# Kernel optimization log

Measured on AMD Instinct MI355X. Metric: run time of the kernel, lower is better.

The kernel has to match this reference:

```python
import jax, jax.numpy as jnp
import numpy as np

PI_2 = 3.14159 / 2  # matches torch module constant (not exact pi/2, keeps tan finite)
EPS_SUM = 1e-07
EPS_COS = 1e-08  # torch F.cosine_similarity default eps


def setup_inputs() -> dict:
    key = jax.random.key(0)
    k1, k2 = jax.random.split(key)
    B, N, C, H, W = 16, 2000, 512, 7, 7
    # memory is uniform-initialized then sum-normalized per cube, as in __init__
    memory = jax.random.uniform(k1, (N, C, H, W), dtype=jnp.float32)
    memory = memory / (jnp.sum(memory, axis=(1, 2, 3), keepdims=True) + EPS_SUM)
    key_t = jax.random.uniform(k2, (B, C, H, W), dtype=jnp.float32)
    return {"key": key_t, "memory": memory}


def reference(key, memory):
    # _normalize: divide key by its per-sample sum
    k = key / (jnp.sum(key, axis=(1, 2, 3), keepdims=True) + EPS_SUM)
    B = k.shape[0]
    N = memory.shape[0]
    kf = k.reshape(B, -1)            # [B, D], D = C*H*W
    mf = memory.reshape(N, -1)       # [N, D]
    # cosine similarity (torch clamps each norm to eps)
    dots = jnp.einsum('bd,nd->bn', kf, mf)                       # [B, N]
    kn = jnp.maximum(jnp.linalg.norm(kf, axis=-1), EPS_COS)      # [B]
    mn = jnp.maximum(jnp.linalg.norm(mf, axis=-1), EPS_COS)      # [N]
    cos = dots / (kn[:, None] * mn[None, :])
    w = jax.nn.softmax(jnp.tan(cos * PI_2), axis=1)              # [B, N]
    # read: sum over memory cubes weighted by address w
    return jnp.einsum('bn,nchw->bchw', w, memory)                # [B, C, H, W]
```

## Files before the change

### kernel.cpp

```cpp
#include <hip/hip_runtime.h>
#include <hip/hip_fp16.h>
#include <math.h>

#define B 16
#define N 2000
#define D 25088
#define D4 6272
#define PI2 1.570795f
#define KC 28
#define KSPAN (D / KC)
#define KTILES (KSPAN / 32)
#define NT (D / 32)
#define KBLK (NT / 4)
#define NCHUNK 20
#define NPER (N / NCHUNK)
#define SELHI 0x07060302u
#define PSCALE 1048576.0f
#define PINV   (1.0f / 1048576.0f)

typedef __attribute__((ext_vector_type(8))) short short8;
typedef __attribute__((ext_vector_type(4))) float f32x4;
typedef unsigned int uint;

union pk { uint4 u; short8 s; };
__device__ __forceinline__ short8 as_s8(uint4 u) { pk p; p.u = u; return p.s; }
union hpk { __half2 h; uint u; };

__device__ __forceinline__ float wave_sum(float v) {
#pragma unroll
    for (int off = 32; off > 0; off >>= 1) v += __shfl_xor(v, off, 64);
    return v;
}
__device__ __forceinline__ float wave_max(float v) {
#pragma unroll
    for (int off = 32; off > 0; off >>= 1) v = fmaxf(v, __shfl_xor(v, off, 64));
    return v;
}

__device__ __forceinline__ void cvt_hilo(const float4& a, const float4& b,
                                         short8& hi, short8& lo, float4& msqv) {
    float xs[8] = {a.x, a.y, a.z, a.w, b.x, b.y, b.z, b.w};
    float* mq = &msqv.x;
    uint lu[8];
#pragma unroll
    for (int j = 0; j < 8; ++j) {
        uint u = __float_as_uint(xs[j]);
        float lof = xs[j] - __uint_as_float(u & 0xffff0000u);
        lu[j] = __float_as_uint(lof);
        mq[j & 3] = fmaf(xs[j], xs[j], mq[j & 3]);
    }
    uint4 h, l;
    h.x = __builtin_amdgcn_perm(__float_as_uint(xs[1]), __float_as_uint(xs[0]), SELHI);
    h.y = __builtin_amdgcn_perm(__float_as_uint(xs[3]), __float_as_uint(xs[2]), SELHI);
    h.z = __builtin_amdgcn_perm(__float_as_uint(xs[5]), __float_as_uint(xs[4]), SELHI);
    h.w = __builtin_amdgcn_perm(__float_as_uint(xs[7]), __float_as_uint(xs[6]), SELHI);
    l.x = __builtin_amdgcn_perm(lu[1], lu[0], SELHI);
    l.y = __builtin_amdgcn_perm(lu[3], lu[2], SELHI);
    l.z = __builtin_amdgcn_perm(lu[5], lu[4], SELHI);
    l.w = __builtin_amdgcn_perm(lu[7], lu[6], SELHI);
    hi = as_s8(h); lo = as_s8(l);
}

__global__ void k_split(const float* __restrict__ key, unsigned short* __restrict__ ksw,
                        float* __restrict__ zdst, float* __restrict__ kpart) {
    const int tid  = threadIdx.x;
    const int bx   = blockIdx.x;
    const int g    = bx * 256 + tid;
    if (g < B * N + N) zdst[g] = 0.f;
    const int tile = g >> 6, lane = g & 63;
    const int m = lane & 15, quad = lane >> 4;
    const float* src = key + (size_t)m * D + tile * 32 + quad * 8;
    float4 x0 = *(const float4*)src;
    float4 x1 = *(const float4*)(src + 4);
    short8 hi, lo;
    float4 msqv = {0.f, 0.f, 0.f, 0.f};
    cvt_hilo(x0, x1, hi, lo, msqv);
    pk ph; ph.s = hi;
    pk pl; pl.s = lo;
    *(uint4*)(ksw + ((size_t)tile * 64 + lane) * 8)        = ph.u;
    *(uint4*)(ksw + ((size_t)(NT + tile) * 64 + lane) * 8) = pl.u;

    float ssq = (msqv.x + msqv.y) + (msqv.z + msqv.w);
    ssq += __shfl_xor(ssq, 16, 64);
    ssq += __shfl_xor(ssq, 32, 64);
    __shared__ float lds[4][16];
    if (quad == 0) lds[tid >> 6][m] = ssq;
    __syncthreads();
    if (tid < 16)
        kpart[bx * 16 + tid] = lds[0][tid] + lds[1][tid] + lds[2][tid] + lds[3][tid];
}

__global__ __launch_bounds__(256, 3) void k_dots(const float* __restrict__ mem,
                                                 const unsigned short* __restrict__ ksw,
                                                 float* __restrict__ dots,
                                                 float* __restrict__ mn2) {
    const int tid  = threadIdx.x;
    const int lane = tid & 63;
    const int wave = tid >> 6;
    const int n0   = blockIdx.x * 16;
    const int kc   = blockIdx.y * 4 + wave;
    const int nrow = lane & 15, quad = lane >> 4;

    const float4* mrow4 = (const float4*)(mem + (size_t)(n0 + nrow) * D + kc * KSPAN) + quad * 2;
    const uint4* khp = (const uint4*)(ksw + ((size_t)(kc * KTILES) * 64 + lane) * 8);
    const uint4* klp = (const uint4*)(ksw + ((size_t)(NT + kc * KTILES) * 64 + lane) * 8);

    f32x4 ahh = {0.f, 0.f, 0.f, 0.f};
    f32x4 ahl = ahh, alh = ahh;
    float4 msqv = {0.f, 0.f, 0.f, 0.f};

    float4 a0 = mrow4[0], a1 = mrow4[1];
    uint4  ha = khp[0],   la = klp[0];
    float4 b0 = mrow4[8], b1 = mrow4[9];
    uint4  hb = khp[64],  lb = klp[64];

    for (int t = 0; t < KTILES; t += 2) {
        const int t2 = (t + 2 < KTILES) ? t + 2 : t;
        const int t3 = (t + 3 < KTILES) ? t + 3 : t;
        float4 na0 = mrow4[(size_t)t2 * 8], na1 = mrow4[(size_t)t2 * 8 + 1];
        uint4  nha = khp[(size_t)t2 * 64],  nla = klp[(size_t)t2 * 64];
        float4 nb0 = mrow4[(size_t)t3 * 8], nb1 = mrow4[(size_t)t3 * 8 + 1];
        uint4  nhb = khp[(size_t)t3 * 64],  nlb = klp[(size_t)t3 * 64];

        short8 bh, bl;
        cvt_hilo(a0, a1, bh, bl, msqv);
        {
            short8 kh = as_s8(ha), kl = as_s8(la);
            ahh = __builtin_amdgcn_mfma_f32_16x16x32_bf16(kh, bh, ahh, 0, 0, 0);
            ahl = __builtin_amdgcn_mfma_f32_16x16x32_bf16(kh, bl, ahl, 0, 0, 0);
            alh = __builtin_amdgcn_mfma_f32_16x16x32_bf16(kl, bh, alh, 0, 0, 0);
        }
        cvt_hilo(b0, b1, bh, bl, msqv);
        {
            short8 kh = as_s8(hb), kl = as_s8(lb);
            ahh = __builtin_amdgcn_mfma_f32_16x16x32_bf16(kh, bh, ahh, 0, 0, 0);
            ahl = __builtin_amdgcn_mfma_f32_16x16x32_bf16(kh, bl, ahl, 0, 0, 0);
            alh = __builtin_amdgcn_mfma_f32_16x16x32_bf16(kl, bh, alh, 0, 0, 0);
        }
        a0 = na0; a1 = na1; ha = nha; la = nla;
        b0 = nb0; b1 = nb1; hb = nhb; lb = nlb;
    }

#pragma unroll
    for (int r = 0; r < 4; ++r)
        unsafeAtomicAdd(&dots[(size_t)(quad * 4 + r) * N + n0 + nrow],
                        ahh[r] + ahl[r] + alh[r]);

    float msq = (msqv.x + msqv.y) + (msqv.z + msqv.w);
    msq += __shfl_xor(msq, 16, 64);
    msq += __shfl_xor(msq, 32, 64);
    if (quad == 0) unsafeAtomicAdd(&mn2[n0 + nrow], msq);
}

__global__ __launch_bounds__(256, 2) void k_softmax(const float* __restrict__ kpart,
                                                    const float* __restrict__ dots,
                                                    const float* __restrict__ mn2,
                                                    float* __restrict__ w) {
    const int b = blockIdx.x, tid = threadIdx.x;
    const int wv = tid >> 6, ln = tid & 63;
    __shared__ float t[N];
    __shared__ float redB[4], redC[4];

    float s = (tid < KBLK) ? kpart[tid * 16 + b] : 0.f;
    s = wave_sum(s);
    if (ln == 0) redB[wv] = s;
    __syncthreads();
    const float kn = fmaxf(sqrtf(redB[0] + redB[1] + redB[2] + redB[3]), 1e-8f);
    __syncthreads();

    float mx = -1e30f;
    for (int n = tid; n < N; n += 256) {
        float mn = fmaxf(sqrtf(mn2[n]), 1e-8f);
        float tv = tanf(dots[(size_t)b * N + n] / (kn * mn) * PI2);
        t[n] = tv;
        mx = fmaxf(mx, tv);
    }
    mx = wave_max(mx);
    if (ln == 0) redB[wv] = mx;
    __syncthreads();
    mx = fmaxf(fmaxf(redB[0], redB[1]), fmaxf(redB[2], redB[3]));

    float sum = 0.f;
    for (int n = tid; n < N; n += 256) {
        float e = expf(t[n] - mx);
        t[n] = e;
        sum += e;
    }
    sum = wave_sum(sum);
    if (ln == 0) redC[wv] = sum;
    __syncthreads();
    sum = redC[0] + redC[1] + redC[2] + redC[3];
    const float inv = 1.f / sum;
    for (int n = tid; n < N; n += 256) w[(size_t)b * N + n] = t[n] * inv;
}

__global__ __launch_bounds__(256, 4) void k_out_p(const float4* __restrict__ mem,
                                                  const float* __restrict__ w,
                                                  uint2* __restrict__ part) {
    const int tid = threadIdx.x;
    const int d4  = blockIdx.x * 256 + tid;
    const int n0  = blockIdx.y * NPER;

    __shared__ float wt[B * NPER];
    for (int i = tid; i < B * NPER; i += 256)
        wt[i] = w[(size_t)(i / NPER) * N + n0 + (i % NPER)];
    __syncthreads();
    if (d4 >= D4) return;

    const float4* mp = mem + (size_t)n0 * D4 + d4;
    float4 acc[B];
#pragma unroll
    for (int b = 0; b < B; ++b) acc[b] = make_float4(0.f, 0.f, 0.f, 0.f);

    float4 cur[4];
#pragma unroll
    for (int u = 0; u < 4; ++u) cur[u] = mp[(size_t)u * D4];

    for (int g = 0; g < NPER / 4; ++g) {
        const int gn = (g + 1 < NPER / 4) ? g + 1 : g;
        float4 nxt[4];
#pragma unroll
        for (int u = 0; u < 4; ++u) nxt[u] = mp[(size_t)(gn * 4 + u) * D4];
#pragma unroll
        for (int b = 0; b < B; ++b) {
            const float4 wv = *((const float4*)(wt + b * NPER) + g);
            float4 a = acc[b];
            a.x = fmaf(wv.x, cur[0].x, a.x); a.y = fmaf(wv.x, cur[0].y, a.y);
            a.z = fmaf(wv.x, cur[0].z, a.z); a.w = fmaf(wv.x, cur[0].w, a.w);
            a.x = fmaf(wv.y, cur[1].x, a.x); a.y = fmaf(wv.y, cur[1].y, a.y);
            a.z = fmaf(wv.y, cur[1].z, a.z); a.w = fmaf(wv.y, cur[1].w, a.w);
            a.x = fmaf(wv.z, cur[2].x, a.x); a.y = fmaf(wv.z, cur[2].y, a.y);
            a.z = fmaf(wv.z, cur[2].z, a.z); a.w = fmaf(wv.z, cur[2].w, a.w);
            a.x = fmaf(wv.w, cur[3].x, a.x); a.y = fmaf(wv.w, cur[3].y, a.y);
            a.z = fmaf(wv.w, cur[3].z, a.z); a.w = fmaf(wv.w, cur[3].w, a.w);
            acc[b] = a;
        }
#pragma unroll
        for (int u = 0; u < 4; ++u) cur[u] = nxt[u];
    }
#pragma unroll
    for (int b = 0; b < B; ++b) {
        hpk p0, p1;
        p0.h = __floats2half2_rn(acc[b].x * PSCALE, acc[b].y * PSCALE);
        p1.h = __floats2half2_rn(acc[b].z * PSCALE, acc[b].w * PSCALE);
        uint2 v; v.x = p0.u; v.y = p1.u;
        part[((size_t)blockIdx.y * B + b) * D4 + d4] = v;
    }
}

__global__ void k_reduce(const uint2* __restrict__ part, float4* __restrict__ out) {
    const int i = blockIdx.x * 256 + threadIdx.x;
    float sx = 0.f, sy = 0.f, sz = 0.f, sw = 0.f;
#pragma unroll
    for (int c = 0; c < NCHUNK; ++c) {
        uint2 v = part[(size_t)c * B * D4 + i];
        hpk a, b2; a.u = v.x; b2.u = v.y;
        float2 f0 = __half22float2(a.h), f1 = __half22float2(b2.h);
        sx += f0.x; sy += f0.y; sz += f1.x; sw += f1.y;
    }
    out[i] = make_float4(sx * PINV, sy * PINV, sz * PINV, sw * PINV);
}

__global__ __launch_bounds__(256, 2) void k_out_atomic(const float4* __restrict__ mem,
                                                       const float* __restrict__ w,
                                                       float* __restrict__ out) {
    const int tid = threadIdx.x;
    const int d4  = blockIdx.x * 256 + tid;
    const int n0  = blockIdx.y * NPER;
    __shared__ float wt[B * NPER];
    for (int i = tid; i < B * NPER; i += 256)
        wt[i] = w[(size_t)(i / NPER) * N + n0 + (i % NPER)];
    __syncthreads();
    if (d4 >= D4) return;
    const float4* mp = mem + (size_t)n0 * D4 + d4;
    float4 acc[B];
#pragma unroll
    for (int b = 0; b < B; ++b) acc[b] = make_float4(0.f, 0.f, 0.f, 0.f);
    for (int n = 0; n < NPER; n += 4) {
        float4 mv[4];
#pragma unroll
        for (int u = 0; u < 4; ++u) mv[u] = mp[(size_t)(n + u) * D4];
#pragma unroll
        for (int b = 0; b < B; ++b) {
            float4 a = acc[b];
#pragma unroll
            for (int u = 0; u < 4; ++u) {
                const float wv = wt[b * NPER + n + u];
                a.x = fmaf(wv, mv[u].x, a.x); a.y = fmaf(wv, mv[u].y, a.y);
                a.z = fmaf(wv, mv[u].z, a.z); a.w = fmaf(wv, mv[u].w, a.w);
            }
            acc[b] = a;
        }
    }
#pragma unroll
    for (int b = 0; b < B; ++b) {
        float* op = out + (size_t)b * D + (size_t)d4 * 4;
        unsafeAtomicAdd(op + 0, acc[b].x);
        unsafeAtomicAdd(op + 1, acc[b].y);
        unsafeAtomicAdd(op + 2, acc[b].z);
        unsafeAtomicAdd(op + 3, acc[b].w);
    }
}

extern "C" void kernel_launch(void* const* d_in, const int* in_sizes, int n_in,
                              void* d_out, int out_size, void* d_ws, size_t ws_size,
                              hipStream_t stream) {
    const float* key = (const float*)d_in[0];
    const float* mem = (const float*)d_in[1];
    float* out = (float*)d_out;

    float* ws = (float*)d_ws;
    unsigned short* ksw = (unsigned short*)ws;
    float* dots  = ws + 401408;
    float* mn2   = dots + (size_t)B * N;
    float* kpart = mn2 + N;
    float* w     = kpart + (size_t)KBLK * 16;
    float* part  = w + (size_t)B * N;
    const size_t need_full =
        (size_t)(401408 + B * N + N + KBLK * 16 + B * N + (size_t)NCHUNK * B * D4 * 2) * 4;

    k_split<<<dim3(KBLK), 256, 0, stream>>>(key, ksw, dots, kpart);
    k_dots<<<dim3(N / 16, KC / 4), 256, 0, stream>>>(mem, ksw, dots, mn2);
    k_softmax<<<dim3(B), 256, 0, stream>>>(kpart, dots, mn2, w);
    if (ws_size >= need_full) {
        k_out_p<<<dim3((D4 + 255) / 256, NCHUNK), 256, 0, stream>>>((const float4*)mem, w, (uint2*)part);
        k_reduce<<<dim3(B * D4 / 256), 256, 0, stream>>>((const uint2*)part, (float4*)out);
    } else {
        hipMemsetAsync(d_out, 0, (size_t)B * D * sizeof(float), stream);
        k_out_atomic<<<dim3((D4 + 255) / 256, NCHUNK), 256, 0, stream>>>((const float4*)mem, w, out);
    }
}
```

Before: 332.4 us.

## Fuse softmax into chunked output kernel using per-chunk max and sum rescaling

Removes the separate single-pass softmax kernel, which used only 16 blocks. Each output-chunk block now computes tan(cos) and a local softmax for its 100-row slice. It writes per-chunk max and partition sums, and the reduce kernel rescales each chunk's partial sum with a flash-attention style combine. This drops a serial, low-occupancy launch but repeats the tan/exp and norm work in every block along x. Chunk-local exp values are stored as scaled fp16 partials, which can shift precision.

```diff
diff --git a/kernel.cpp b/kernel.cpp
--- a/kernel.cpp
+++ b/kernel.cpp
@@ -152,6 +152,139 @@
     if (quad == 0) unsafeAtomicAdd(&mn2[n0 + nrow], msq);
 }
 
+__global__ __launch_bounds__(256, 4) void k_out_p(const float4* __restrict__ mem,
+                                                  const float* __restrict__ dots,
+                                                  const float* __restrict__ mn2,
+                                                  const float* __restrict__ kpart,
+                                                  uint2* __restrict__ part,
+                                                  float2* __restrict__ meta) {
+    const int tid = threadIdx.x;
+    const int d4  = blockIdx.x * 256 + tid;
+    const int c   = blockIdx.y;
+    const int n0  = c * NPER;
+    const int lane = tid & 63, wv = tid >> 6;
+
+    __shared__ float wt[B * NPER];
+    __shared__ float sknp[16][16];
+    __shared__ float skn[16];
+    __shared__ float smn[NPER];
+    __shared__ float mxs[16], Zs[16];
+
+    {
+        float s = 0.f;
+        for (int j = tid >> 4; j < KBLK; j += 16) s += kpart[j * 16 + (tid & 15)];
+        sknp[tid >> 4][tid & 15] = s;
+    }
+    for (int i = tid; i < NPER; i += 256) smn[i] = fmaxf(sqrtf(mn2[n0 + i]), 1e-8f);
+    __syncthreads();
+    if (tid < 16) {
+        float s = 0.f;
+#pragma unroll
+        for (int j = 0; j < 16; ++j) s += sknp[j][tid];
+        skn[tid] = fmaxf(sqrtf(s), 1e-8f);
+    }
+    __syncthreads();
+
+    for (int i = tid; i < B * NPER; i += 256) {
+        const int b = i / NPER, n = i % NPER;
+        wt[i] = tanf(dots[(size_t)b * N + n0 + n] / (skn[b] * smn[n]) * PI2);
+    }
+    __syncthreads();
+
+#pragma unroll
+    for (int j = 0; j < 4; ++j) {
+        const int b = wv + 4 * j;
+        float v0 = wt[b * NPER + lane];
+        float v1 = (lane + 64 < NPER) ? wt[b * NPER + lane + 64] : -1e30f;
+        float mx = wave_max(fmaxf(v0, v1));
+        float e0 = expf(v0 - mx);
+        float e1 = (lane + 64 < NPER) ? expf(v1 - mx) : 0.f;
+        wt[b * NPER + lane] = e0;
+        if (lane + 64 < NPER) wt[b * NPER + lane + 64] = e1;
+        float Z = wave_sum(e0 + e1);
+        if (lane == 0) { mxs[b] = mx; Zs[b] = Z; }
+    }
+    __syncthreads();
+    if (blockIdx.x == 0 && tid < 16) meta[c * 16 + tid] = make_float2(mxs[tid], Zs[tid]);
+    if (d4 >= D4) return;
+
+    const float4* mp = mem + (size_t)n0 * D4 + d4;
+    float4 acc[B];
+#pragma unroll
+    for (int b = 0; b < B; ++b) acc[b] = make_float4(0.f, 0.f, 0.f, 0.f);
+
+    float4 cur[4];
+#pragma unroll
+    for (int u = 0; u < 4; ++u) cur[u] = mp[(size_t)u * D4];
+
+    for (int g = 0; g < NPER / 4; ++g) {
+        const int gn = (g + 1 < NPER / 4) ? g + 1 : g;
+        float4 nxt[4];
+#pragma unroll
+        for (int u = 0; u < 4; ++u) nxt[u] = mp[(size_t)(gn * 4 + u) * D4];
+#pragma unroll
+        for (int b = 0; b < B; ++b) {
+            const float4 wv4 = *((const float4*)(wt + b * NPER) + g);
+            float4 a = acc[b];
+            a.x = fmaf(wv4.x, cur[0].x, a.x); a.y = fmaf(wv4.x, cur[0].y, a.y);
+            a.z = fmaf(wv4.x, cur[0].z, a.z); a.w = fmaf(wv4.x, cur[0].w, a.w);
+            a.x = fmaf(wv4.y, cur[1].x, a.x); a.y = fmaf(wv4.y, cur[1].y, a.y);
+            a.z = fmaf(wv4.y, cur[1].z, a.z); a.w = fmaf(wv4.y, cur[1].w, a.w);
+            a.x = fmaf(wv4.z, cur[2].x, a.x); a.y = fmaf(wv4.z, cur[2].y, a.y);
+            a.z = fmaf(wv4.z, cur[2].z, a.z); a.w = fmaf(wv4.z, cur[2].w, a.w);
+            a.x = fmaf(wv4.w, cur[3].x, a.x); a.y = fmaf(wv4.w, cur[3].y, a.y);
+            a.z = fmaf(wv4.w, cur[3].z, a.z); a.w = fmaf(wv4.w, cur[3].w, a.w);
+            acc[b] = a;
+        }
+#pragma unroll
+        for (int u = 0; u < 4; ++u) cur[u] = nxt[u];
+    }
+#pragma unroll
+    for (int b = 0; b < B; ++b) {
+        hpk p0, p1;
+        p0.h = __floats2half2_rn(acc[b].x * PSCALE, acc[b].y * PSCALE);
+        p1.h = __floats2half2_rn(acc[b].z * PSCALE, acc[b].w * PSCALE);
+        uint2 v; v.x = p0.u; v.y = p1.u;
+        part[((size_t)c * B + b) * D4 + d4] = v;
+    }
+}
+
+__global__ void k_reduce(const uint2* __restrict__ part, const float2* __restrict__ meta,
+                         float4* __restrict__ out) {
+    const int tid = threadIdx.x;
+    __shared__ float2 smeta[NCHUNK * 16];
+    __shared__ float scl[NCHUNK * 16];
+    for (int j = tid; j < NCHUNK * 16; j += 256) smeta[j] = meta[j];
+    __syncthreads();
+    if (tid < 16) {
+        float MX = -1e30f;
+#pragma unroll
+        for (int c = 0; c < NCHUNK; ++c) MX = fmaxf(MX, smeta[c * 16 + tid].x);
+        float den = 0.f;
+#pragma unroll
+        for (int c = 0; c < NCHUNK; ++c)
+            den += expf(smeta[c * 16 + tid].x - MX) * smeta[c * 16 + tid].y;
+        const float inv = 1.f / den;
+#pragma unroll
+        for (int c = 0; c < NCHUNK; ++c)
+            scl[c * 16 + tid] = expf(smeta[c * 16 + tid].x - MX) * inv;
+    }
+    __syncthreads();
+    const int i = blockIdx.x * 256 + tid;
+    const int b = i / D4;
+    float sx = 0.f, sy = 0.f, sz = 0.f, sw = 0.f;
+#pragma unroll
+    for (int c = 0; c < NCHUNK; ++c) {
+        uint2 v = part[(size_t)c * B * D4 + i];
+        hpk a, b2; a.u = v.x; b2.u = v.y;
+        float2 f0 = __half22float2(a.h), f1 = __half22float2(b2.h);
+        const float sc = scl[c * 16 + b];
+        sx = fmaf(sc, f0.x, sx); sy = fmaf(sc, f0.y, sy);
+        sz = fmaf(sc, f1.x, sz); sw = fmaf(sc, f1.y, sw);
+    }
+    out[i] = make_float4(sx * PINV, sy * PINV, sz * PINV, sw * PINV);
+}
+
 __global__ __launch_bounds__(256, 2) void k_softmax(const float* __restrict__ kpart,
                                                     const float* __restrict__ dots,
                                                     const float* __restrict__ mn2,
@@ -192,73 +325,6 @@
     sum = redC[0] + redC[1] + redC[2] + redC[3];
     const float inv = 1.f / sum;
     for (int n = tid; n < N; n += 256) w[(size_t)b * N + n] = t[n] * inv;
-}
-
-__global__ __launch_bounds__(256, 4) void k_out_p(const float4* __restrict__ mem,
-                                                  const float* __restrict__ w,
-                                                  uint2* __restrict__ part) {
-    const int tid = threadIdx.x;
-    const int d4  = blockIdx.x * 256 + tid;
-    const int n0  = blockIdx.y * NPER;
-
-    __shared__ float wt[B * NPER];
-    for (int i = tid; i < B * NPER; i += 256)
-        wt[i] = w[(size_t)(i / NPER) * N + n0 + (i % NPER)];
-    __syncthreads();
-    if (d4 >= D4) return;
-
-    const float4* mp = mem + (size_t)n0 * D4 + d4;
-    float4 acc[B];
-#pragma unroll
-    for (int b = 0; b < B; ++b) acc[b] = make_float4(0.f, 0.f, 0.f, 0.f);
-
-    float4 cur[4];
-#pragma unroll
-    for (int u = 0; u < 4; ++u) cur[u] = mp[(size_t)u * D4];
-
-    for (int g = 0; g < NPER / 4; ++g) {
-        const int gn = (g + 1 < NPER / 4) ? g + 1 : g;
-        float4 nxt[4];
-#pragma unroll
-        for (int u = 0; u < 4; ++u) nxt[u] = mp[(size_t)(gn * 4 + u) * D4];
-#pragma unroll
-        for (int b = 0; b < B; ++b) {
-            const float4 wv = *((const float4*)(wt + b * NPER) + g);
-            float4 a = acc[b];
-            a.x = fmaf(wv.x, cur[0].x, a.x); a.y = fmaf(wv.x, cur[0].y, a.y);
-            a.z = fmaf(wv.x, cur[0].z, a.z); a.w = fmaf(wv.x, cur[0].w, a.w);
-            a.x = fmaf(wv.y, cur[1].x, a.x); a.y = fmaf(wv.y, cur[1].y, a.y);
-            a.z = fmaf(wv.y, cur[1].z, a.z); a.w = fmaf(wv.y, cur[1].w, a.w);
-            a.x = fmaf(wv.z, cur[2].x, a.x); a.y = fmaf(wv.z, cur[2].y, a.y);
-            a.z = fmaf(wv.z, cur[2].z, a.z); a.w = fmaf(wv.z, cur[2].w, a.w);
-            a.x = fmaf(wv.w, cur[3].x, a.x); a.y = fmaf(wv.w, cur[3].y, a.y);
-            a.z = fmaf(wv.w, cur[3].z, a.z); a.w = fmaf(wv.w, cur[3].w, a.w);
-            acc[b] = a;
-        }
-#pragma unroll
-        for (int u = 0; u < 4; ++u) cur[u] = nxt[u];
-    }
-#pragma unroll
-    for (int b = 0; b < B; ++b) {
-        hpk p0, p1;
-        p0.h = __floats2half2_rn(acc[b].x * PSCALE, acc[b].y * PSCALE);
-        p1.h = __floats2half2_rn(acc[b].z * PSCALE, acc[b].w * PSCALE);
-        uint2 v; v.x = p0.u; v.y = p1.u;
-        part[((size_t)blockIdx.y * B + b) * D4 + d4] = v;
-    }
-}
-
-__global__ void k_reduce(const uint2* __restrict__ part, float4* __restrict__ out) {
-    const int i = blockIdx.x * 256 + threadIdx.x;
-    float sx = 0.f, sy = 0.f, sz = 0.f, sw = 0.f;
-#pragma unroll
-    for (int c = 0; c < NCHUNK; ++c) {
-        uint2 v = part[(size_t)c * B * D4 + i];
-        hpk a, b2; a.u = v.x; b2.u = v.y;
-        float2 f0 = __half22float2(a.h), f1 = __half22float2(b2.h);
-        sx += f0.x; sy += f0.y; sz += f1.x; sw += f1.y;
-    }
-    out[i] = make_float4(sx * PINV, sy * PINV, sz * PINV, sw * PINV);
 }
 
 __global__ __launch_bounds__(256, 2) void k_out_atomic(const float4* __restrict__ mem,
@@ -314,18 +380,22 @@
     float* dots  = ws + 401408;
     float* mn2   = dots + (size_t)B * N;
     float* kpart = mn2 + N;
-    float* w     = kpart + (size_t)KBLK * 16;
+    float* meta  = kpart + (size_t)KBLK * 16;
+    float* w     = meta + (size_t)NCHUNK * 16 * 2;
     float* part  = w + (size_t)B * N;
     const size_t need_full =
-        (size_t)(401408 + B * N + N + KBLK * 16 + B * N + (size_t)NCHUNK * B * D4 * 2) * 4;
+        (size_t)(401408 + B * N + N + KBLK * 16 + NCHUNK * 32 + B * N
+                 + (size_t)NCHUNK * B * D4 * 2) * 4;
 
     k_split<<<dim3(KBLK), 256, 0, stream>>>(key, ksw, dots, kpart);
     k_dots<<<dim3(N / 16, KC / 4), 256, 0, stream>>>(mem, ksw, dots, mn2);
-    k_softmax<<<dim3(B), 256, 0, stream>>>(kpart, dots, mn2, w);
     if (ws_size >= need_full) {
-        k_out_p<<<dim3((D4 + 255) / 256, NCHUNK), 256, 0, stream>>>((const float4*)mem, w, (uint2*)part);
-        k_reduce<<<dim3(B * D4 / 256), 256, 0, stream>>>((const uint2*)part, (float4*)out);
+        k_out_p<<<dim3((D4 + 255) / 256, NCHUNK), 256, 0, stream>>>(
+            (const float4*)mem, dots, mn2, kpart, (uint2*)part, (float2*)meta);
+        k_reduce<<<dim3(B * D4 / 256), 256, 0, stream>>>((const uint2*)part,
+                                                         (const float2*)meta, (float4*)out);
     } else {
+        k_softmax<<<dim3(B), 256, 0, stream>>>(kpart, dots, mn2, w);
         hipMemsetAsync(d_out, 0, (size_t)B * D * sizeof(float), stream);
         k_out_atomic<<<dim3((D4 + 255) / 256, NCHUNK), 256, 0, stream>>>((const float4*)mem, w, out);
     }
```

Result: no change. 332.3 us (-0.0%).
